# Kernel optimization log

Measured on AMD Instinct MI355X. Metric: run time of the kernel, lower is better.

Reference implementation:

```python
import jax, jax.numpy as jnp
import numpy as np

B, T, D, H, Dh = 2, 2048, 2048, 16, 128


def setup_inputs() -> dict:
    key = jax.random.key(0)
    ks = jax.random.split(key, 9)
    s = 0.02
    return {
        "x": jax.random.normal(ks[0], (B, T, D), jnp.float32),
        "Wq": jax.random.normal(ks[1], (H, D, Dh), jnp.float32) * s,
        "bq": jax.random.normal(ks[2], (H, Dh), jnp.float32) * s,
        "Wk": jax.random.normal(ks[3], (H, D, Dh), jnp.float32) * s,
        "bk": jax.random.normal(ks[4], (H, Dh), jnp.float32) * s,
        "Wv": jax.random.normal(ks[5], (H, D, Dh), jnp.float32) * s,
        "bv": jax.random.normal(ks[6], (H, Dh), jnp.float32) * s,
        "Wp": jax.random.normal(ks[7], (D, D), jnp.float32) * s,
        "bp": jax.random.normal(ks[8], (D,), jnp.float32) * s,
    }


def reference(x, Wq, bq, Wk, bk, Wv, bv, Wp, bp):
    # per-head projections (stacked): [B, H, T, Dh]
    q = jnp.einsum("btd,hde->bhte", x, Wq) + bq[None, :, None, :]
    k = jnp.einsum("btd,hde->bhte", x, Wk) + bk[None, :, None, :]
    v = jnp.einsum("btd,hde->bhte", x, Wv) + bv[None, :, None, :]
    scale = Dh ** -0.5
    att = jnp.einsum("bhte,bhse->bhts", q, k) * scale  # [B,H,T,T]
    causal = jnp.tril(jnp.ones((T, T), bool))
    att = jnp.where(causal, att, -jnp.inf)
    att = jax.nn.softmax(att, axis=-1)
    # dropout p=0.0 -> identity
    out = jnp.einsum("bhts,bhse->bhte", att, v)  # [B,H,T,Dh]
    out = out.transpose(0, 2, 1, 3).reshape(B, T, H * Dh)  # concat heads
    return out @ Wp.T if False else jnp.einsum("btd,ed->bte", out, Wp.T) if False else out @ Wp + bp
```

## Files before the change

kernel.cpp:

```cpp
#include <hip/hip_runtime.h>
#include <hip/hip_bf16.h>
#include <math.h>

typedef __attribute__((ext_vector_type(8))) short bf16x8;
typedef __attribute__((ext_vector_type(4))) float f32x4;
typedef __attribute__((ext_vector_type(16))) float f32x16;

__device__ __forceinline__ unsigned short f2b(float f) {
    union { float f; unsigned u; } a; a.f = f;
    unsigned r = a.u + 0x7FFFu + ((a.u >> 16) & 1u);
    return (unsigned short)(r >> 16);
}

__device__ __forceinline__ void gl_lds16(const unsigned short* g, unsigned short* l) {
    __builtin_amdgcn_global_load_lds(
        (const __attribute__((address_space(1))) unsigned int*)g,
        (__attribute__((address_space(3))) unsigned int*)l,
        16, 0, 0);
}

#define SCALE2 0.12751744716529944f

__global__ __launch_bounds__(256) void cast_x_kernel(const float* __restrict__ x,
                                                     unsigned short* __restrict__ xb, int n4) {
    int i = blockIdx.x * 256 + threadIdx.x;
    if (i >= n4) return;
    float4 v = ((const float4*)x)[i];
    ushort4 o;
    o.x = f2b(v.x); o.y = f2b(v.y); o.z = f2b(v.z); o.w = f2b(v.w);
    ((ushort4*)xb)[i] = o;
}

__global__ __launch_bounds__(256) void transpose_cast_kernel(const float* __restrict__ in,
                                                             unsigned short* __restrict__ out,
                                                             int R, int C) {
    __shared__ float tile[32][33];
    int c0 = blockIdx.x * 32, r0 = blockIdx.y * 32;
    int tx = threadIdx.x, ty = threadIdx.y;
#pragma unroll
    for (int i = 0; i < 32; i += 8)
        tile[ty + i][tx] = in[(size_t)(r0 + ty + i) * C + c0 + tx];
    __syncthreads();
#pragma unroll
    for (int i = 0; i < 32; i += 8)
        out[(size_t)(c0 + ty + i) * R + r0 + tx] = f2b(tile[tx][ty + i]);
}

__global__ __launch_bounds__(256) void transpose_cast3_kernel(const float* __restrict__ Wq,
                                                              const float* __restrict__ Wk,
                                                              const float* __restrict__ Wv,
                                                              unsigned short* __restrict__ out) {
    __shared__ float tile[32][33];
    int z = blockIdx.z;
    int mat = z >> 4, hh = z & 15;
    const float* src = ((mat == 0) ? Wq : (mat == 1) ? Wk : Wv) + (size_t)hh * 2048 * 128;
    unsigned short* dst = out + (size_t)z * 128 * 2048;
    int c0 = blockIdx.x * 32, r0 = blockIdx.y * 32;
    int tx = threadIdx.x, ty = threadIdx.y;
#pragma unroll
    for (int i = 0; i < 32; i += 8)
        tile[ty + i][tx] = src[(size_t)(r0 + ty + i) * 128 + c0 + tx];
    __syncthreads();
#pragma unroll
    for (int i = 0; i < 32; i += 8)
        dst[(size_t)(c0 + ty + i) * 2048 + r0 + tx] = f2b(tile[tx][ty + i]);
}

constexpr int BKg = 64;

__global__ __launch_bounds__(256) void qkv_gemm_kernel(
    const unsigned short* __restrict__ xb,
    const unsigned short* __restrict__ wt,
    const float* __restrict__ bq, const float* __restrict__ bkb, const float* __restrict__ bvb,
    unsigned short* __restrict__ q, unsigned short* __restrict__ k, unsigned short* __restrict__ vt) {
    __shared__ unsigned short sA[128 * 64];
    __shared__ unsigned short sB[128 * 64];
    int cb = blockIdx.x;
    int m0 = blockIdx.y * 128;
    int tid = threadIdx.x;
    int lane = tid & 63, w = tid >> 6;
    int wm = w >> 1, wn = w & 1;
    int l32 = lane & 31, kh = lane >> 5;
    int srow = lane >> 3;
    int gcol = ((lane & 7) ^ srow) * 8;
    int swz = l32 & 7;

    f32x16 acc[2][2] = {};
    const unsigned short* aBase = xb + (size_t)m0 * 2048;
    const unsigned short* bBase = wt + (size_t)cb * 128 * 2048;

    for (int k0 = 0; k0 < 2048; k0 += BKg) {
#pragma unroll
        for (int p = 0; p < 4; ++p) {
            int row = w * 32 + p * 8 + srow;
            gl_lds16(aBase + (size_t)row * 2048 + k0 + gcol, sA + (w * 32 + p * 8) * 64);
            gl_lds16(bBase + (size_t)row * 2048 + k0 + gcol, sB + (w * 32 + p * 8) * 64);
        }
        __syncthreads();
#pragma unroll
        for (int kst = 0; kst < 4; ++kst) {
            int chunk = kst * 2 + kh;
            bf16x8 af[2], bfr[2];
#pragma unroll
            for (int a = 0; a < 2; ++a)
                af[a] = *(const bf16x8*)(sA + (wm * 64 + a * 32 + l32) * 64 + (chunk ^ swz) * 8);
#pragma unroll
            for (int b = 0; b < 2; ++b)
                bfr[b] = *(const bf16x8*)(sB + (wn * 64 + b * 32 + l32) * 64 + (chunk ^ swz) * 8);
#pragma unroll
            for (int a = 0; a < 2; ++a)
#pragma unroll
                for (int b = 0; b < 2; ++b)
                    acc[a][b] = __builtin_amdgcn_mfma_f32_32x32x16_bf16(af[a], bfr[b], acc[a][b], 0, 0, 0);
        }
        __syncthreads();
    }

    int mat = cb >> 4, h = cb & 15;
    const float* bias = (mat == 0) ? bq : (mat == 1) ? bkb : bvb;
    unsigned short* outqk = (mat == 0) ? q : k;
    float postscale = (mat == 0) ? SCALE2 : 1.0f;
#pragma unroll
    for (int a = 0; a < 2; ++a) {
#pragma unroll
        for (int b = 0; b < 2; ++b) {
            int col = wn * 64 + b * 32 + l32;
            float bb = bias[h * 128 + col];
            if (mat < 2) {
#pragma unroll
                for (int reg = 0; reg < 16; ++reg) {
                    int gr = m0 + wm * 64 + a * 32 + (reg & 3) + 8 * (reg >> 2) + 4 * kh;
                    int bi = gr >> 11, t = gr & 2047;
                    outqk[((size_t)(bi * 16 + h) * 2048 + t) * 128 + col] =
                        f2b((acc[a][b][reg] + bb) * postscale);
                }
            } else {
#pragma unroll
                for (int rg = 0; rg < 4; ++rg) {
                    int gr = m0 + wm * 64 + a * 32 + 8 * rg + 4 * kh;
                    int bi = gr >> 11, t = gr & 2047;
                    ushort4 pk;
                    pk.x = f2b(acc[a][b][rg * 4 + 0] + bb);
                    pk.y = f2b(acc[a][b][rg * 4 + 1] + bb);
                    pk.z = f2b(acc[a][b][rg * 4 + 2] + bb);
                    pk.w = f2b(acc[a][b][rg * 4 + 3] + bb);
                    *(ushort4*)(vt + ((size_t)(bi * 16 + h) * 128 + col) * 2048 + t) = pk;
                }
            }
        }
    }
}

__global__ __launch_bounds__(256) void attn_kernel(
    const unsigned short* __restrict__ qg,
    const unsigned short* __restrict__ kg,
    const unsigned short* __restrict__ vg,
    unsigned short* __restrict__ og) {
    constexpr int LDP = 72;
    __shared__ unsigned short sK[64 * 128];
    __shared__ unsigned short sV[128 * 64];
    __shared__ unsigned short sP[4 * 16 * LDP];

    int bh = blockIdx.x;
    int t0 = (31 - (int)blockIdx.y) * 64;
    int tid = threadIdx.x;
    int lane = tid & 63, w = tid >> 6;
    int ln = lane & 15, quad = lane >> 4;
    int swz = ln & 7;

    const unsigned short* qb = qg + (size_t)bh * 2048 * 128;
    const unsigned short* kb = kg + (size_t)bh * 2048 * 128;
    const unsigned short* vb = vg + (size_t)bh * 128 * 2048;

    bf16x8 qf[4];
#pragma unroll
    for (int c = 0; c < 4; ++c)
        qf[c] = *(const bf16x8*)(qb + (size_t)(t0 + w * 16 + ln) * 128 + c * 32 + quad * 8);

    f32x4 oacc[8] = {};
    float mst[4], lst[4];
#pragma unroll
    for (int r = 0; r < 4; ++r) { mst[r] = -INFINITY; lst[r] = 0.f; }

    int nblk = t0 / 64 + 1;

    int kr = lane >> 4, km = lane & 15;
    int vr = lane >> 3, vm = lane & 7;

    for (int jb = 0; jb < nblk; ++jb) {
        int s0 = jb * 64;
#pragma unroll
        for (int p = 0; p < 4; ++p) {
            int krow = w * 16 + p * 4;
            int rswk = (krow + kr) & 7;
            int kch = (km & 8) | ((km & 7) ^ rswk);
            gl_lds16(kb + (size_t)(s0 + krow + kr) * 128 + kch * 8, sK + krow * 128);
            int vrow = w * 32 + p * 8;
            int vch = vm ^ vr;
            gl_lds16(vb + (size_t)(vrow + vr) * 2048 + s0 + vch * 8, sV + vrow * 64);
        }
        __syncthreads();
        {
            f32x4 sacc[4] = {};
#pragma unroll
            for (int c = 0; c < 4; ++c) {
                bf16x8 bfr[4];
#pragma unroll
                for (int j = 0; j < 4; ++j) {
                    int ch = c * 4 + quad;
                    int pos = (ch & 8) | ((ch ^ swz) & 7);
                    bfr[j] = *(const bf16x8*)(sK + (j * 16 + ln) * 128 + pos * 8);
                }
#pragma unroll
                for (int j = 0; j < 4; ++j)
                    sacc[j] = __builtin_amdgcn_mfma_f32_16x16x32_bf16(qf[c], bfr[j], sacc[j], 0, 0, 0);
            }
#pragma unroll
            for (int r = 0; r < 4; ++r) {
                int t = t0 + w * 16 + quad * 4 + r;
                float pv[4];
                float rm = -INFINITY;
#pragma unroll
                for (int j = 0; j < 4; ++j) {
                    int s = s0 + j * 16 + ln;
                    float vv = sacc[j][r];
                    if (s > t) vv = -INFINITY;
                    pv[j] = vv;
                    rm = fmaxf(rm, vv);
                }
#pragma unroll
                for (int m_ = 8; m_ >= 1; m_ >>= 1)
                    rm = fmaxf(rm, __shfl_xor(rm, m_, 64));
                float mnew = fmaxf(mst[r], rm);
                float alpha = exp2f(mst[r] - mnew);
                float rsum = 0.f;
#pragma unroll
                for (int j = 0; j < 4; ++j) {
                    float p_ = exp2f(pv[j] - mnew);
                    rsum += p_;
                    sP[(w * 16 + quad * 4 + r) * LDP + j * 16 + ln] = f2b(p_);
                }
#pragma unroll
                for (int m_ = 8; m_ >= 1; m_ >>= 1)
                    rsum += __shfl_xor(rsum, m_, 64);
                lst[r] = lst[r] * alpha + rsum;
                mst[r] = mnew;
#pragma unroll
                for (int jj = 0; jj < 8; ++jj)
                    oacc[jj][r] *= alpha;
            }
#pragma unroll
            for (int c2 = 0; c2 < 2; ++c2) {
                bf16x8 af, bfr[8];
                af = *(const bf16x8*)(sP + (w * 16 + ln) * LDP + c2 * 32 + quad * 8);
#pragma unroll
                for (int jj = 0; jj < 8; ++jj) {
                    int pos = (c2 * 4 + quad) ^ swz;
                    bfr[jj] = *(const bf16x8*)(sV + (jj * 16 + ln) * 64 + pos * 8);
                }
#pragma unroll
                for (int jj = 0; jj < 8; ++jj)
                    oacc[jj] = __builtin_amdgcn_mfma_f32_16x16x32_bf16(af, bfr[jj], oacc[jj], 0, 0, 0);
            }
        }
        __syncthreads();
    }

#pragma unroll
    for (int r = 0; r < 4; ++r) {
        int t = t0 + w * 16 + quad * 4 + r;
        float inv = 1.f / lst[r];
#pragma unroll
        for (int jj = 0; jj < 8; ++jj) {
            int e = jj * 16 + ln;
            og[((size_t)bh * 2048 + t) * 128 + e] = f2b(oacc[jj][r] * inv);
        }
    }
}

__global__ __launch_bounds__(256) void proj_gemm_kernel(
    const unsigned short* __restrict__ og,
    const unsigned short* __restrict__ wpt,
    const float* __restrict__ bp,
    float* __restrict__ out) {
    __shared__ unsigned short sA[128 * 64];
    __shared__ unsigned short sB[128 * 64];
    int cb = blockIdx.x;
    int m0 = blockIdx.y * 128;
    int b_ = m0 >> 11, t0_ = m0 & 2047;
    int tid = threadIdx.x;
    int lane = tid & 63, w = tid >> 6;
    int wm = w >> 1, wn = w & 1;
    int l32 = lane & 31, kh = lane >> 5;
    int srow = lane >> 3;
    int gcol = ((lane & 7) ^ srow) * 8;
    int swz = l32 & 7;

    f32x16 acc[2][2] = {};
    const unsigned short* bBase = wpt + (size_t)cb * 128 * 2048;

    for (int k0 = 0; k0 < 2048; k0 += BKg) {
        int h = k0 >> 7, e0 = k0 & 127;
        const unsigned short* aBase = og + ((size_t)(b_ * 16 + h) * 2048 + t0_) * 128 + e0;
#pragma unroll
        for (int p = 0; p < 4; ++p) {
            int row = w * 32 + p * 8 + srow;
            gl_lds16(aBase + (size_t)row * 128 + gcol, sA + (w * 32 + p * 8) * 64);
            gl_lds16(bBase + (size_t)row * 2048 + k0 + gcol, sB + (w * 32 + p * 8) * 64);
        }
        __syncthreads();
#pragma unroll
        for (int kst = 0; kst < 4; ++kst) {
            int chunk = kst * 2 + kh;
            bf16x8 af[2], bfr[2];
#pragma unroll
            for (int a = 0; a < 2; ++a)
                af[a] = *(const bf16x8*)(sA + (wm * 64 + a * 32 + l32) * 64 + (chunk ^ swz) * 8);
#pragma unroll
            for (int b = 0; b < 2; ++b)
                bfr[b] = *(const bf16x8*)(sB + (wn * 64 + b * 32 + l32) * 64 + (chunk ^ swz) * 8);
#pragma unroll
            for (int a = 0; a < 2; ++a)
#pragma unroll
                for (int b = 0; b < 2; ++b)
                    acc[a][b] = __builtin_amdgcn_mfma_f32_32x32x16_bf16(af[a], bfr[b], acc[a][b], 0, 0, 0);
        }
        __syncthreads();
    }

#pragma unroll
    for (int a = 0; a < 2; ++a)
#pragma unroll
        for (int b = 0; b < 2; ++b) {
            int col = cb * 128 + wn * 64 + b * 32 + l32;
            float bias = bp[col];
#pragma unroll
            for (int reg = 0; reg < 16; ++reg) {
                int row = m0 + wm * 64 + a * 32 + (reg & 3) + 8 * (reg >> 2) + 4 * kh;
                out[(size_t)row * 2048 + col] = acc[a][b][reg] + bias;
            }
        }
}

extern "C" void kernel_launch(void* const* d_in, const int* in_sizes, int n_in,
                              void* d_out, int out_size, void* d_ws, size_t ws_size,
                              hipStream_t stream) {
    const float* x  = (const float*)d_in[0];
    const float* Wq = (const float*)d_in[1];
    const float* bq = (const float*)d_in[2];
    const float* Wk = (const float*)d_in[3];
    const float* bk = (const float*)d_in[4];
    const float* Wv = (const float*)d_in[5];
    const float* bv = (const float*)d_in[6];
    const float* Wp = (const float*)d_in[7];
    const float* bp = (const float*)d_in[8];
    float* out = (float*)d_out;

    char* ws = (char*)d_ws;
    unsigned short* xb  = (unsigned short*)(ws);
    unsigned short* wt  = (unsigned short*)(ws + 16777216);
    unsigned short* wpt = (unsigned short*)(ws + 41943040);
    unsigned short* q   = (unsigned short*)(ws + 50331648);
    unsigned short* k   = (unsigned short*)(ws + 67108864);
    unsigned short* vt  = (unsigned short*)(ws + 83886080);
    unsigned short* o   = (unsigned short*)(ws + 100663296);

    cast_x_kernel<<<8192, 256, 0, stream>>>(x, xb, 2097152);
    dim3 tb(32, 8);
    transpose_cast3_kernel<<<dim3(4, 64, 48), tb, 0, stream>>>(Wq, Wk, Wv, wt);
    transpose_cast_kernel<<<dim3(64, 64, 1), tb, 0, stream>>>(Wp, wpt, 2048, 2048);
    qkv_gemm_kernel<<<dim3(48, 32), 256, 0, stream>>>(xb, wt, bq, bk, bv, q, k, vt);
    attn_kernel<<<dim3(32, 32), 256, 0, stream>>>(q, k, vt, o);
    proj_gemm_kernel<<<dim3(16, 32), 256, 0, stream>>>(o, wpt, bp, out);
}
```

Measured before the change: 413.0 us.

## Double-buffer attention K/V tiles, mask only diagonal block, fuse prep kernels

Three preprocessing kernels (x cast, QKV weight transpose, Wp transpose) are merged into one launch, cutting launch overhead. The attention kernel now double-buffers K/V tiles in LDS, so the next block's global-to-LDS loads overlap compute on the current one, with one barrier per iteration. The causal mask is applied only on the diagonal block, and the per-row sum shuffle reduction is deferred to the epilogue, which removes shuffles from the inner loop. LDS use for K/V doubles, which may lower occupancy.

```diff
diff --git a/kernel.cpp b/kernel.cpp
--- a/kernel.cpp
+++ b/kernel.cpp
@@ -21,49 +21,50 @@
 
 #define SCALE2 0.12751744716529944f
 
-__global__ __launch_bounds__(256) void cast_x_kernel(const float* __restrict__ x,
-                                                     unsigned short* __restrict__ xb, int n4) {
-    int i = blockIdx.x * 256 + threadIdx.x;
-    if (i >= n4) return;
-    float4 v = ((const float4*)x)[i];
-    ushort4 o;
-    o.x = f2b(v.x); o.y = f2b(v.y); o.z = f2b(v.z); o.w = f2b(v.w);
-    ((ushort4*)xb)[i] = o;
-}
-
-__global__ __launch_bounds__(256) void transpose_cast_kernel(const float* __restrict__ in,
-                                                             unsigned short* __restrict__ out,
-                                                             int R, int C) {
-    __shared__ float tile[32][33];
-    int c0 = blockIdx.x * 32, r0 = blockIdx.y * 32;
+__global__ __launch_bounds__(256) void prep_kernel(
+    const float* __restrict__ x,
+    const float* __restrict__ Wq, const float* __restrict__ Wk,
+    const float* __restrict__ Wv, const float* __restrict__ Wp,
+    unsigned short* __restrict__ xb, unsigned short* __restrict__ wt,
+    unsigned short* __restrict__ wpt) {
+    __shared__ float tile_s[32][33];
+    int bid = blockIdx.x;
     int tx = threadIdx.x, ty = threadIdx.y;
-#pragma unroll
-    for (int i = 0; i < 32; i += 8)
-        tile[ty + i][tx] = in[(size_t)(r0 + ty + i) * C + c0 + tx];
-    __syncthreads();
-#pragma unroll
-    for (int i = 0; i < 32; i += 8)
-        out[(size_t)(c0 + ty + i) * R + r0 + tx] = f2b(tile[tx][ty + i]);
-}
-
-__global__ __launch_bounds__(256) void transpose_cast3_kernel(const float* __restrict__ Wq,
-                                                              const float* __restrict__ Wk,
-                                                              const float* __restrict__ Wv,
-                                                              unsigned short* __restrict__ out) {
-    __shared__ float tile[32][33];
-    int z = blockIdx.z;
-    int mat = z >> 4, hh = z & 15;
-    const float* src = ((mat == 0) ? Wq : (mat == 1) ? Wk : Wv) + (size_t)hh * 2048 * 128;
-    unsigned short* dst = out + (size_t)z * 128 * 2048;
-    int c0 = blockIdx.x * 32, r0 = blockIdx.y * 32;
-    int tx = threadIdx.x, ty = threadIdx.y;
-#pragma unroll
-    for (int i = 0; i < 32; i += 8)
-        tile[ty + i][tx] = src[(size_t)(r0 + ty + i) * 128 + c0 + tx];
-    __syncthreads();
-#pragma unroll
-    for (int i = 0; i < 32; i += 8)
-        dst[(size_t)(c0 + ty + i) * 2048 + r0 + tx] = f2b(tile[tx][ty + i]);
+    if (bid < 12288) {
+        int z = bid >> 8;
+        int tile = bid & 255;
+        int c0 = (tile & 3) * 32, r0 = (tile >> 2) * 32;
+        int mat = z >> 4, hh = z & 15;
+        const float* src = ((mat == 0) ? Wq : (mat == 1) ? Wk : Wv) + (size_t)hh * 2048 * 128;
+        unsigned short* dst = wt + (size_t)z * 128 * 2048;
+#pragma unroll
+        for (int i = 0; i < 32; i += 8)
+            tile_s[ty + i][tx] = src[(size_t)(r0 + ty + i) * 128 + c0 + tx];
+        __syncthreads();
+#pragma unroll
+        for (int i = 0; i < 32; i += 8)
+            dst[(size_t)(c0 + ty + i) * 2048 + r0 + tx] = f2b(tile_s[tx][ty + i]);
+    } else if (bid < 16384) {
+        int tile = bid - 12288;
+        int c0 = (tile & 63) * 32, r0 = (tile >> 6) * 32;
+#pragma unroll
+        for (int i = 0; i < 32; i += 8)
+            tile_s[ty + i][tx] = Wp[(size_t)(r0 + ty + i) * 2048 + c0 + tx];
+        __syncthreads();
+#pragma unroll
+        for (int i = 0; i < 32; i += 8)
+            wpt[(size_t)(c0 + ty + i) * 2048 + r0 + tx] = f2b(tile_s[tx][ty + i]);
+    } else {
+        int base = (bid - 16384) * 1024 + ty * 32 + tx;
+#pragma unroll
+        for (int rep = 0; rep < 4; ++rep) {
+            int i = base + rep * 256;
+            float4 v = ((const float4*)x)[i];
+            ushort4 o;
+            o.x = f2b(v.x); o.y = f2b(v.y); o.z = f2b(v.z); o.w = f2b(v.w);
+            ((ushort4*)xb)[i] = o;
+        }
+    }
 }
 
 constexpr int BKg = 64;
@@ -157,8 +158,8 @@
     const unsigned short* __restrict__ vg,
     unsigned short* __restrict__ og) {
     constexpr int LDP = 72;
-    __shared__ unsigned short sK[64 * 128];
-    __shared__ unsigned short sV[128 * 64];
+    __shared__ unsigned short sK[2][64 * 128];
+    __shared__ unsigned short sV[2][128 * 64];
     __shared__ unsigned short sP[4 * 16 * LDP];
 
     int bh = blockIdx.x;
@@ -187,89 +188,107 @@
     int kr = lane >> 4, km = lane & 15;
     int vr = lane >> 3, vm = lane & 7;
 
-    for (int jb = 0; jb < nblk; ++jb) {
-        int s0 = jb * 64;
+    {
+        int s0 = 0;
 #pragma unroll
         for (int p = 0; p < 4; ++p) {
             int krow = w * 16 + p * 4;
             int rswk = (krow + kr) & 7;
             int kch = (km & 8) | ((km & 7) ^ rswk);
-            gl_lds16(kb + (size_t)(s0 + krow + kr) * 128 + kch * 8, sK + krow * 128);
+            gl_lds16(kb + (size_t)(s0 + krow + kr) * 128 + kch * 8, sK[0] + krow * 128);
             int vrow = w * 32 + p * 8;
             int vch = vm ^ vr;
-            gl_lds16(vb + (size_t)(vrow + vr) * 2048 + s0 + vch * 8, sV + vrow * 64);
-        }
-        __syncthreads();
-        {
-            f32x4 sacc[4] = {};
-#pragma unroll
-            for (int c = 0; c < 4; ++c) {
-                bf16x8 bfr[4];
-#pragma unroll
-                for (int j = 0; j < 4; ++j) {
-                    int ch = c * 4 + quad;
-                    int pos = (ch & 8) | ((ch ^ swz) & 7);
-                    bfr[j] = *(const bf16x8*)(sK + (j * 16 + ln) * 128 + pos * 8);
-                }
-#pragma unroll
-                for (int j = 0; j < 4; ++j)
-                    sacc[j] = __builtin_amdgcn_mfma_f32_16x16x32_bf16(qf[c], bfr[j], sacc[j], 0, 0, 0);
-            }
-#pragma unroll
-            for (int r = 0; r < 4; ++r) {
-                int t = t0 + w * 16 + quad * 4 + r;
-                float pv[4];
-                float rm = -INFINITY;
-#pragma unroll
-                for (int j = 0; j < 4; ++j) {
-                    int s = s0 + j * 16 + ln;
-                    float vv = sacc[j][r];
-                    if (s > t) vv = -INFINITY;
-                    pv[j] = vv;
-                    rm = fmaxf(rm, vv);
-                }
-#pragma unroll
-                for (int m_ = 8; m_ >= 1; m_ >>= 1)
-                    rm = fmaxf(rm, __shfl_xor(rm, m_, 64));
-                float mnew = fmaxf(mst[r], rm);
-                float alpha = exp2f(mst[r] - mnew);
-                float rsum = 0.f;
-#pragma unroll
-                for (int j = 0; j < 4; ++j) {
-                    float p_ = exp2f(pv[j] - mnew);
-                    rsum += p_;
-                    sP[(w * 16 + quad * 4 + r) * LDP + j * 16 + ln] = f2b(p_);
-                }
-#pragma unroll
-                for (int m_ = 8; m_ >= 1; m_ >>= 1)
-                    rsum += __shfl_xor(rsum, m_, 64);
-                lst[r] = lst[r] * alpha + rsum;
-                mst[r] = mnew;
-#pragma unroll
-                for (int jj = 0; jj < 8; ++jj)
-                    oacc[jj][r] *= alpha;
-            }
-#pragma unroll
-            for (int c2 = 0; c2 < 2; ++c2) {
-                bf16x8 af, bfr[8];
-                af = *(const bf16x8*)(sP + (w * 16 + ln) * LDP + c2 * 32 + quad * 8);
-#pragma unroll
-                for (int jj = 0; jj < 8; ++jj) {
-                    int pos = (c2 * 4 + quad) ^ swz;
-                    bfr[jj] = *(const bf16x8*)(sV + (jj * 16 + ln) * 64 + pos * 8);
-                }
-#pragma unroll
-                for (int jj = 0; jj < 8; ++jj)
-                    oacc[jj] = __builtin_amdgcn_mfma_f32_16x16x32_bf16(af, bfr[jj], oacc[jj], 0, 0, 0);
-            }
-        }
-        __syncthreads();
+            gl_lds16(vb + (size_t)(vrow + vr) * 2048 + s0 + vch * 8, sV[0] + vrow * 64);
+        }
+    }
+
+    for (int jb = 0; jb < nblk; ++jb) {
+        int s0 = jb * 64;
+        int buf = jb & 1;
+        __syncthreads();
+        if (jb + 1 < nblk) {
+            int s1 = s0 + 64;
+#pragma unroll
+            for (int p = 0; p < 4; ++p) {
+                int krow = w * 16 + p * 4;
+                int rswk = (krow + kr) & 7;
+                int kch = (km & 8) | ((km & 7) ^ rswk);
+                gl_lds16(kb + (size_t)(s1 + krow + kr) * 128 + kch * 8, sK[buf ^ 1] + krow * 128);
+                int vrow = w * 32 + p * 8;
+                int vch = vm ^ vr;
+                gl_lds16(vb + (size_t)(vrow + vr) * 2048 + s1 + vch * 8, sV[buf ^ 1] + vrow * 64);
+            }
+        }
+        bool diag = (jb == nblk - 1);
+
+        f32x4 sacc[4] = {};
+#pragma unroll
+        for (int c = 0; c < 4; ++c) {
+            bf16x8 bfr[4];
+#pragma unroll
+            for (int j = 0; j < 4; ++j) {
+                int ch = c * 4 + quad;
+                int pos = (ch & 8) | ((ch ^ swz) & 7);
+                bfr[j] = *(const bf16x8*)(sK[buf] + (j * 16 + ln) * 128 + pos * 8);
+            }
+#pragma unroll
+            for (int j = 0; j < 4; ++j)
+                sacc[j] = __builtin_amdgcn_mfma_f32_16x16x32_bf16(qf[c], bfr[j], sacc[j], 0, 0, 0);
+        }
+#pragma unroll
+        for (int r = 0; r < 4; ++r) {
+            int t = t0 + w * 16 + quad * 4 + r;
+            float pv[4];
+            float rm = -INFINITY;
+#pragma unroll
+            for (int j = 0; j < 4; ++j) {
+                float vv = sacc[j][r];
+                if (diag) { if (s0 + j * 16 + ln > t) vv = -INFINITY; }
+                pv[j] = vv;
+                rm = fmaxf(rm, vv);
+            }
+#pragma unroll
+            for (int m_ = 8; m_ >= 1; m_ >>= 1)
+                rm = fmaxf(rm, __shfl_xor(rm, m_, 64));
+            float mnew = fmaxf(mst[r], rm);
+            float alpha = exp2f(mst[r] - mnew);
+            float p0 = exp2f(pv[0] - mnew);
+            float p1 = exp2f(pv[1] - mnew);
+            float p2 = exp2f(pv[2] - mnew);
+            float p3 = exp2f(pv[3] - mnew);
+            sP[(w * 16 + quad * 4 + r) * LDP + 0 * 16 + ln] = f2b(p0);
+            sP[(w * 16 + quad * 4 + r) * LDP + 1 * 16 + ln] = f2b(p1);
+            sP[(w * 16 + quad * 4 + r) * LDP + 2 * 16 + ln] = f2b(p2);
+            sP[(w * 16 + quad * 4 + r) * LDP + 3 * 16 + ln] = f2b(p3);
+            lst[r] = lst[r] * alpha + (p0 + p1) + (p2 + p3);
+            mst[r] = mnew;
+#pragma unroll
+            for (int jj = 0; jj < 8; ++jj)
+                oacc[jj][r] *= alpha;
+        }
+#pragma unroll
+        for (int c2 = 0; c2 < 2; ++c2) {
+            bf16x8 af, bfr[8];
+            af = *(const bf16x8*)(sP + (w * 16 + ln) * LDP + c2 * 32 + quad * 8);
+#pragma unroll
+            for (int jj = 0; jj < 8; ++jj) {
+                int pos = (c2 * 4 + quad) ^ swz;
+                bfr[jj] = *(const bf16x8*)(sV[buf] + (jj * 16 + ln) * 64 + pos * 8);
+            }
+#pragma unroll
+            for (int jj = 0; jj < 8; ++jj)
+                oacc[jj] = __builtin_amdgcn_mfma_f32_16x16x32_bf16(af, bfr[jj], oacc[jj], 0, 0, 0);
+        }
     }
 
 #pragma unroll
     for (int r = 0; r < 4; ++r) {
         int t = t0 + w * 16 + quad * 4 + r;
-        float inv = 1.f / lst[r];
+        float lsum = lst[r];
+#pragma unroll
+        for (int m_ = 8; m_ >= 1; m_ >>= 1)
+            lsum += __shfl_xor(lsum, m_, 64);
+        float inv = 1.f / lsum;
 #pragma unroll
         for (int jj = 0; jj < 8; ++jj) {
             int e = jj * 16 + ln;
@@ -365,10 +384,8 @@
     unsigned short* vt  = (unsigned short*)(ws + 83886080);
     unsigned short* o   = (unsigned short*)(ws + 100663296);
 
-    cast_x_kernel<<<8192, 256, 0, stream>>>(x, xb, 2097152);
     dim3 tb(32, 8);
-    transpose_cast3_kernel<<<dim3(4, 64, 48), tb, 0, stream>>>(Wq, Wk, Wv, wt);
-    transpose_cast_kernel<<<dim3(64, 64, 1), tb, 0, stream>>>(Wp, wpt, 2048, 2048);
+    prep_kernel<<<18432, tb, 0, stream>>>(x, Wq, Wk, Wv, Wp, xb, wt, wpt);
     qkv_gemm_kernel<<<dim3(48, 32), 256, 0, stream>>>(xb, wt, bq, bk, bv, q, k, vt);
     attn_kernel<<<dim3(32, 32), 256, 0, stream>>>(q, k, vt, o);
     proj_gemm_kernel<<<dim3(16, 32), 256, 0, stream>>>(o, wpt, bp, out);
```

New measurement: 390.4 us. 5.5% less time.
